# Performance work log

Measured on AMD Instinct MI355X. Metric: run time of the kernel, lower is better.

Reference implementation:

```python
import jax, jax.numpy as jnp
import numpy as np

B, I, O, C, U = 32, 2048, 32, 16, 32  # batch, in_channels(caps), out_capsules, in_capsules(dim), unit_size
NUM_ITERS = 3


def setup_inputs() -> dict:
    key = jax.random.key(0)
    k1, k2 = jax.random.split(key)
    x = jax.random.normal(k1, (B, I, C), dtype=jnp.float32)
    w = jax.random.normal(k2, (I, O, C, U), dtype=jnp.float32)
    return {"x": x, "w": w}


def _squash(v):
    # faithful to original: vec * |vec| / (1 + |vec|^2), norm over last (unit) dim
    n = jnp.linalg.norm(v, axis=-1, keepdims=True)
    return v * n / (1.0 + n * n)


def reference(x, w):
    # u_hat[b,i,o,u] = sum_c x[b,i,c] * w[i,o,c,u]   (the original's x @ w with singleton dims dropped)
    u_hat = jnp.einsum('bic,iocu->biou', x, w)  # [B,I,O,U]
    b_log = jnp.zeros((I, O, 1), dtype=x.dtype)
    v = None
    for _ in range(NUM_ITERS):
        # original computes softmax over dim=2 of [I,O,1] (a singleton dim) -> all ones; kept faithful
        c = jax.nn.softmax(b_log, axis=2)[..., 0]  # [I,O]
        s = jnp.einsum('io,biou->bou', c, u_hat)   # sum over input capsules
        v = _squash(s)                              # [B,O,U]
        # agreement: per-(b,i,o) dot(u_hat, v), then mean over batch (original's update.mean(dim=0))
        agree = jnp.einsum('biou,bou->io', u_hat, v) / B
        b_log = b_log + agree[..., None]
    return v[:, :, None, :]  # matches original v.squeeze(1) -> [B, O, 1, U]
```

## Files before the change

### kernel.cpp

```cpp
#include <hip/hip_runtime.h>
#include <math.h>

#define B_   32
#define I_   2048
#define O_   32
#define C_   16
#define U_   32
#define NCOL (O_ * U_)

#define TI   4
#define OQ_  4
#define OB_  (O_ / OQ_)
#define NIH  (I_ / TI)
#define NBLK (NIH * OQ_)
#define SLICE (B_ * OB_ * U_)
#define XS   36


__global__ __launch_bounds__(256, 8) void caps_partial(const float* __restrict__ x,
                                                       const float* __restrict__ w,
                                                       float* __restrict__ ws) {
    __shared__ float xs[TI * C_ * XS];
    const int tid = threadIdx.x;
    const int ih  = blockIdx.x & (NIH - 1);
    const int oq  = blockIdx.x >> 9;
    const int i0  = ih * TI;
    const int o0  = oq * OB_;

    for (int k = tid; k < B_ * TI * C_; k += 256) {
        int b   = k >> 6;
        int rem = k & 63;
        xs[rem * XS + b] = x[(size_t)b * (I_ * C_) + (size_t)i0 * C_ + rem];
    }
    __syncthreads();

    const int bh = tid >> 6;
    const int ct = tid & 63;
    const int oo = ct >> 3;
    const int u4 = (ct & 7) << 2;
    const float* wp = w + (size_t)i0 * (O_ * C_ * U_) + (size_t)(o0 + oo) * (C_ * U_) + u4;

    float4 acc[8];
#pragma unroll
    for (int b = 0; b < 8; ++b) acc[b] = make_float4(0.f, 0.f, 0.f, 0.f);

    for (int il = 0; il < TI; ++il) {
        const float* wpi = wp + (size_t)il * (O_ * C_ * U_);
        const float* xr  = &xs[(il * C_) * XS + bh * 8];
#pragma unroll
        for (int c = 0; c < C_; ++c) {
            float4 wv = *(const float4*)(wpi + c * U_);
            const float4* xv = (const float4*)(xr + c * XS);
            float4 xa = xv[0];
            float4 xb = xv[1];
            acc[0].x = fmaf(xa.x, wv.x, acc[0].x);
            acc[0].y = fmaf(xa.x, wv.y, acc[0].y);
            acc[0].z = fmaf(xa.x, wv.z, acc[0].z);
            acc[0].w = fmaf(xa.x, wv.w, acc[0].w);
            acc[1].x = fmaf(xa.y, wv.x, acc[1].x);
            acc[1].y = fmaf(xa.y, wv.y, acc[1].y);
            acc[1].z = fmaf(xa.y, wv.z, acc[1].z);
            acc[1].w = fmaf(xa.y, wv.w, acc[1].w);
            acc[2].x = fmaf(xa.z, wv.x, acc[2].x);
            acc[2].y = fmaf(xa.z, wv.y, acc[2].y);
            acc[2].z = fmaf(xa.z, wv.z, acc[2].z);
            acc[2].w = fmaf(xa.z, wv.w, acc[2].w);
            acc[3].x = fmaf(xa.w, wv.x, acc[3].x);
            acc[3].y = fmaf(xa.w, wv.y, acc[3].y);
            acc[3].z = fmaf(xa.w, wv.z, acc[3].z);
            acc[3].w = fmaf(xa.w, wv.w, acc[3].w);
            acc[4].x = fmaf(xb.x, wv.x, acc[4].x);
            acc[4].y = fmaf(xb.x, wv.y, acc[4].y);
            acc[4].z = fmaf(xb.x, wv.z, acc[4].z);
            acc[4].w = fmaf(xb.x, wv.w, acc[4].w);
            acc[5].x = fmaf(xb.y, wv.x, acc[5].x);
            acc[5].y = fmaf(xb.y, wv.y, acc[5].y);
            acc[5].z = fmaf(xb.y, wv.z, acc[5].z);
            acc[5].w = fmaf(xb.y, wv.w, acc[5].w);
            acc[6].x = fmaf(xb.z, wv.x, acc[6].x);
            acc[6].y = fmaf(xb.z, wv.y, acc[6].y);
            acc[6].z = fmaf(xb.z, wv.z, acc[6].z);
            acc[6].w = fmaf(xb.z, wv.w, acc[6].w);
            acc[7].x = fmaf(xb.w, wv.x, acc[7].x);
            acc[7].y = fmaf(xb.w, wv.y, acc[7].y);
            acc[7].z = fmaf(xb.w, wv.z, acc[7].z);
            acc[7].w = fmaf(xb.w, wv.w, acc[7].w);
        }
    }

    float* op = ws + (size_t)blockIdx.x * SLICE + (size_t)(bh * 8) * (OB_ * U_)
                + oo * U_ + u4;
#pragma unroll
    for (int bl = 0; bl < 8; ++bl)
        *(float4*)(op + (size_t)bl * (OB_ * U_)) = acc[bl];
}

__global__ __launch_bounds__(256) void caps_reduce_squash(const float* __restrict__ ws,
                                                          float* __restrict__ out) {
    __shared__ float sh[128];
    const int tl = threadIdx.x & 127;
    const int ph = threadIdx.x >> 7;
    const int e  = blockIdx.x * 128 + tl;
    const int b  = e >> 10;
    const int o  = (e >> 5) & 31;
    const int u  = e & 31;
    const int oq = o >> 3;
    const int oo = o & 7;
    const float* p = ws + ((size_t)oq * NIH + (size_t)ph * (NIH / 2)) * SLICE
                     + (size_t)b * (OB_ * U_) + oo * U_ + u;
    float s = 0.f;
#pragma unroll 16
    for (int i = 0; i < NIH / 2; ++i)
        s += p[(size_t)i * SLICE];
    if (ph) sh[tl] = s;
    __syncthreads();
    if (ph == 0) {
        s += sh[tl];
        float ss = s * s;
        ss += __shfl_xor(ss, 1);
        ss += __shfl_xor(ss, 2);
        ss += __shfl_xor(ss, 4);
        ss += __shfl_xor(ss, 8);
        ss += __shfl_xor(ss, 16);
        float n = sqrtf(ss);
        out[e] = s * n / (1.0f + ss);
    }
}

#define FTI 4
__global__ __launch_bounds__(256, 2) void caps_main_atomic(const float* __restrict__ x,
                                                           const float* __restrict__ w,
                                                           float* __restrict__ out) {
    __shared__ float xs[FTI * C_ * 33];
    const int tid = threadIdx.x;
    const int i0 = blockIdx.x * FTI;
    for (int k = tid; k < B_ * FTI * C_; k += 256) {
        int b = k >> 6, rem = k & 63;
        xs[rem * 33 + b] = x[(size_t)b * (I_ * C_) + (size_t)i0 * C_ + rem];
    }
    __syncthreads();
    const int o = tid >> 3, u4 = (tid & 7) << 2;
    const float* wp = w + (size_t)i0 * (O_ * C_ * U_) + o * (C_ * U_) + u4;
    float4 acc[B_];
#pragma unroll
    for (int b = 0; b < B_; ++b) acc[b] = make_float4(0.f, 0.f, 0.f, 0.f);
    for (int il = 0; il < FTI; ++il) {
        const float* wpi = wp + (size_t)il * (O_ * C_ * U_);
        const float* xr = &xs[il * C_ * 33];
#pragma unroll
        for (int c = 0; c < C_; ++c) {
            float4 wv = *(const float4*)(wpi + c * U_);
            const float* xc = xr + c * 33;
#pragma unroll
            for (int b = 0; b < B_; ++b) {
                float xb = xc[b];
                acc[b].x = fmaf(xb, wv.x, acc[b].x);
                acc[b].y = fmaf(xb, wv.y, acc[b].y);
                acc[b].z = fmaf(xb, wv.z, acc[b].z);
                acc[b].w = fmaf(xb, wv.w, acc[b].w);
            }
        }
    }
    float* op = out + o * U_ + u4;
#pragma unroll
    for (int b = 0; b < B_; ++b) {
        float* p = op + (size_t)b * NCOL;
        atomicAdd(p + 0, acc[b].x);
        atomicAdd(p + 1, acc[b].y);
        atomicAdd(p + 2, acc[b].z);
        atomicAdd(p + 3, acc[b].w);
    }
}

__global__ void caps_squash_inplace(float* __restrict__ out) {
    int t = blockIdx.x * 256 + threadIdx.x;
    float s = out[t];
    float ss = s * s;
    ss += __shfl_xor(ss, 1);
    ss += __shfl_xor(ss, 2);
    ss += __shfl_xor(ss, 4);
    ss += __shfl_xor(ss, 8);
    ss += __shfl_xor(ss, 16);
    float n = sqrtf(ss);
    out[t] = s * n / (1.0f + ss);
}

extern "C" void kernel_launch(void* const* d_in, const int* in_sizes, int n_in,
                              void* d_out, int out_size, void* d_ws, size_t ws_size,
                              hipStream_t stream) {
    const float* x = (const float*)d_in[0];
    const float* w = (const float*)d_in[1];
    float* out = (float*)d_out;

    const size_t need = (size_t)NBLK * SLICE * sizeof(float);
    if (ws_size >= need) {
        float* ws = (float*)d_ws;
        caps_partial<<<NBLK, 256, 0, stream>>>(x, w, ws);
        caps_reduce_squash<<<(B_ * NCOL) / 128, 256, 0, stream>>>(ws, out);
    } else {
        hipMemsetAsync(out, 0, (size_t)(B_ * NCOL) * sizeof(float), stream);
        caps_main_atomic<<<I_ / FTI, 256, 0, stream>>>(x, w, out);
        caps_squash_inplace<<<(B_ * NCOL) / 256, 256, 0, stream>>>(out);
    }
}
```

Measured before the change: 229.7 us.

## Stage weights into LDS with double-buffered async global_load_lds and larger tiles

The partial-sum kernel now moves each input capsule's weight slice into double-buffered shared memory using direct global-to-LDS loads. It waits on vmcnt and a barrier so the next slice's load overlaps the current FMA loop, and uses an XOR swizzle to avoid bank conflicts. Tiles grow to 8 input capsules and 16 output capsules per 512-thread block, which halves the partial workspace the reduce kernel has to read. The cost is more LDS per block, lower occupancy and extra barriers.

```diff
diff --git a/kernel.cpp b/kernel.cpp
--- a/kernel.cpp
+++ b/kernel.cpp
@@ -1,5 +1,6 @@
 #include <hip/hip_runtime.h>
 #include <math.h>
+#include <stdint.h>
 
 #define B_   32
 #define I_   2048
@@ -8,51 +9,85 @@
 #define U_   32
 #define NCOL (O_ * U_)
 
-#define TI   4
-#define OQ_  4
-#define OB_  (O_ / OQ_)
+#define TI   8
+#define OSPL 2
+#define OH_  (O_ / OSPL)
 #define NIH  (I_ / TI)
-#define NBLK (NIH * OQ_)
-#define SLICE (B_ * OB_ * U_)
-#define XS   36
-
-
-__global__ __launch_bounds__(256, 8) void caps_partial(const float* __restrict__ x,
+#define NBLK (NIH * OSPL)
+#define SLICE (B_ * OH_ * U_)
+#define WSLH (OH_ * C_ * U_)
+#define XS   32
+
+#define GLOAD_LDS16(gp, lp) \
+    __builtin_amdgcn_global_load_lds( \
+        (const __attribute__((address_space(1))) uint32_t*)(gp), \
+        (__attribute__((address_space(3))) uint32_t*)(lp), 16, 0, 0)
+
+__global__ __launch_bounds__(512, 4) void caps_partial(const float* __restrict__ x,
                                                        const float* __restrict__ w,
                                                        float* __restrict__ ws) {
+    __shared__ float wb[2][WSLH];
     __shared__ float xs[TI * C_ * XS];
     const int tid = threadIdx.x;
     const int ih  = blockIdx.x & (NIH - 1);
-    const int oq  = blockIdx.x >> 9;
+    const int oh  = blockIdx.x >> 8;
     const int i0  = ih * TI;
-    const int o0  = oq * OB_;
-
-    for (int k = tid; k < B_ * TI * C_; k += 256) {
-        int b   = k >> 6;
-        int rem = k & 63;
+    const int o0  = oh * OH_;
+
+    for (int k = tid; k < B_ * TI * C_; k += 512) {
+        int b   = k >> 7;
+        int rem = k & 127;
         xs[rem * XS + b] = x[(size_t)b * (I_ * C_) + (size_t)i0 * C_ + rem];
     }
     __syncthreads();
 
-    const int bh = tid >> 6;
-    const int ct = tid & 63;
-    const int oo = ct >> 3;
-    const int u4 = (ct & 7) << 2;
-    const float* wp = w + (size_t)i0 * (O_ * C_ * U_) + (size_t)(o0 + oo) * (C_ * U_) + u4;
+    const int lane  = tid & 63;
+    const int sbase = tid & ~63;
+
+    auto stage = [&](int il, int buf) {
+        const float* gw = w + (size_t)(i0 + il) * (O_ * C_ * U_);
+        float* lb = &wb[buf][0];
+#pragma unroll
+        for (int k = 0; k < 4; ++k) {
+            int s  = sbase + k * 512 + lane;
+            int o  = s >> 7;
+            int c  = (s >> 3) & 15;
+            int su = s & 7;
+            int src = (o0 + o) * (C_ * U_) + c * U_ + ((su ^ (o & 7)) << 2);
+            GLOAD_LDS16(gw + src, lb + (size_t)s * 4);
+        }
+    };
+
+    const int bh  = tid >> 7;
+    const int ct  = tid & 127;
+    const int oo  = ct >> 3;
+    const int u4i = ct & 7;
+    const int suR = u4i ^ (oo & 7);
 
     float4 acc[8];
 #pragma unroll
-    for (int b = 0; b < 8; ++b) acc[b] = make_float4(0.f, 0.f, 0.f, 0.f);
+    for (int m = 0; m < 8; ++m) acc[m] = make_float4(0.f, 0.f, 0.f, 0.f);
+
+    stage(0, 0);
 
     for (int il = 0; il < TI; ++il) {
-        const float* wpi = wp + (size_t)il * (O_ * C_ * U_);
-        const float* xr  = &xs[(il * C_) * XS + bh * 8];
+        if (il + 1 < TI) {
+            stage(il + 1, (il + 1) & 1);
+            asm volatile("s_waitcnt vmcnt(4)" ::: "memory");
+        } else {
+            asm volatile("s_waitcnt vmcnt(0)" ::: "memory");
+        }
+        __builtin_amdgcn_s_barrier();
+        asm volatile("" ::: "memory");
+
+        const float* cb = &wb[il & 1][oo * (C_ * U_) + suR * 4];
+        const float* xr = &xs[(il * C_) * XS + bh * 8];
 #pragma unroll
         for (int c = 0; c < C_; ++c) {
-            float4 wv = *(const float4*)(wpi + c * U_);
-            const float4* xv = (const float4*)(xr + c * XS);
-            float4 xa = xv[0];
-            float4 xb = xv[1];
+            float4 wv = *(const float4*)(cb + c * U_);
+            const float* xc = xr + c * XS;
+            float4 xa = *(const float4*)(xc);
+            float4 xb = *(const float4*)(xc + 4);
             acc[0].x = fmaf(xa.x, wv.x, acc[0].x);
             acc[0].y = fmaf(xa.x, wv.y, acc[0].y);
             acc[0].z = fmaf(xa.x, wv.z, acc[0].z);
@@ -86,13 +121,16 @@
             acc[7].z = fmaf(xb.w, wv.z, acc[7].z);
             acc[7].w = fmaf(xb.w, wv.w, acc[7].w);
         }
-    }
-
-    float* op = ws + (size_t)blockIdx.x * SLICE + (size_t)(bh * 8) * (OB_ * U_)
-                + oo * U_ + u4;
+
+        asm volatile("" ::: "memory");
+        __builtin_amdgcn_s_barrier();
+    }
+
+    float* op = ws + (size_t)blockIdx.x * SLICE + (size_t)(bh * 8) * (OH_ * U_)
+                + oo * U_ + u4i * 4;
 #pragma unroll
     for (int bl = 0; bl < 8; ++bl)
-        *(float4*)(op + (size_t)bl * (OB_ * U_)) = acc[bl];
+        *(float4*)(op + (size_t)bl * (OH_ * U_)) = acc[bl];
 }
 
 __global__ __launch_bounds__(256) void caps_reduce_squash(const float* __restrict__ ws,
@@ -104,10 +142,10 @@
     const int b  = e >> 10;
     const int o  = (e >> 5) & 31;
     const int u  = e & 31;
-    const int oq = o >> 3;
-    const int oo = o & 7;
-    const float* p = ws + ((size_t)oq * NIH + (size_t)ph * (NIH / 2)) * SLICE
-                     + (size_t)b * (OB_ * U_) + oo * U_ + u;
+    const int oh = o >> 4;
+    const int oo = o & 15;
+    const float* p = ws + ((size_t)oh * NIH + (size_t)ph * (NIH / 2)) * SLICE
+                     + (size_t)b * (OH_ * U_) + oo * U_ + u;
     float s = 0.f;
 #pragma unroll 16
     for (int i = 0; i < NIH / 2; ++i)
@@ -195,7 +233,7 @@
     const size_t need = (size_t)NBLK * SLICE * sizeof(float);
     if (ws_size >= need) {
         float* ws = (float*)d_ws;
-        caps_partial<<<NBLK, 256, 0, stream>>>(x, w, ws);
+        caps_partial<<<NBLK, 512, 0, stream>>>(x, w, ws);
         caps_reduce_squash<<<(B_ * NCOL) / 128, 256, 0, stream>>>(ws, out);
     } else {
         hipMemsetAsync(out, 0, (size_t)(B_ * NCOL) * sizeof(float), stream);
```

Result: faster. 214.4 us (-6.6%).
